# Kernel tuning notes

Hardware: AMD Instinct MI355X
Metric: run time of the kernel (lower is better)

Reference implementation:

```python
import jax, jax.numpy as jnp
import numpy as np

NUM_NEIGHBORS = 3
EPS = 1e-10
B, N1, N2 = 8, 8192, 2048
C1, C2 = 256, 512


def setup_inputs() -> dict:
    key = jax.random.key(0)
    k1, k2, k3, k4 = jax.random.split(key, 4)
    return {
        "query_xyz": jax.random.uniform(k1, (B, 3, N1), dtype=jnp.float32),
        "key_xyz": jax.random.uniform(k2, (B, 3, N2), dtype=jnp.float32),
        "query_feature": jax.random.normal(k3, (B, C1, N1), dtype=jnp.float32),
        "key_feature": jax.random.normal(k4, (B, C2, N2), dtype=jnp.float32),
    }


def reference(query_xyz, key_xyz, query_feature, key_feature):
    # q: (B, N1, 3), k: (B, N2, 3)
    q = jnp.swapaxes(query_xyz, 1, 2)
    k = jnp.swapaxes(key_xyz, 1, 2)
    # squared pairwise distances (B, N1, N2) via ||q||^2 + ||k||^2 - 2 q.k
    d2 = (
        jnp.sum(q * q, axis=-1, keepdims=True)
        + jnp.sum(k * k, axis=-1)[:, None, :]
        - 2.0 * jnp.einsum("bnd,bmd->bnm", q, k)
    )
    # k nearest neighbors (smallest distances)
    neg_d, index = jax.lax.top_k(-d2, NUM_NEIGHBORS)  # (B, N1, K)
    distance = jnp.maximum(-neg_d, EPS)
    inv_distance = 1.0 / distance
    weight = inv_distance / jnp.sum(inv_distance, axis=2, keepdims=True)
    # torch.no_grad() block -> constants w.r.t. autodiff
    weight = jax.lax.stop_gradient(weight)
    index = jax.lax.stop_gradient(index)
    # gather key features: feat_t (B, N2, C2) -> gathered (B, N1, K, C2)
    feat_t = jnp.swapaxes(key_feature, 1, 2)
    batch_idx = jnp.arange(feat_t.shape[0])[:, None, None]
    gathered = feat_t[batch_idx, index]
    # inverse-distance weighted sum -> (B, C2, N1)
    interpolated = jnp.einsum("bnk,bnkc->bcn", weight, gathered)
    return jnp.concatenate([interpolated, query_feature], axis=1)
```

## Files before the change

kernel.cpp:

```cpp
#include <hip/hip_runtime.h>

#define NB 8
#define N1 8192
#define N2 2048
#define C1 256
#define C2 512
#define CO 768
#define CCH 4

typedef float f2 __attribute__((ext_vector_type(2)));
typedef float f4 __attribute__((ext_vector_type(4)));


#define NRM2(X, Y, Z) ({                                                   \
    float _s, _t;                                                          \
    asm("v_mul_f32 %0, %2, %2\n\t"                                         \
        "v_mul_f32 %1, %3, %3\n\t"                                         \
        "v_add_f32 %0, %0, %1\n\t"                                         \
        "v_mul_f32 %1, %4, %4\n\t"                                         \
        "v_add_f32 %0, %0, %1"                                             \
        : "=&v"(_s), "=&v"(_t) : "v"(X), "v"(Y), "v"(Z));                  \
    _s; })

#define PKD2(X01, Y01, Z01, K01, QXD, QYD, QZD, QQD, M2) ({                \
    f2 _d, _s;                                                             \
    asm("v_pk_mul_f32 %0, %2, %6\n\t"           \
        "v_pk_fma_f32 %0, %3, %7, %0\n\t"       \
        "v_pk_fma_f32 %0, %4, %8, %0\n\t"       \
        "v_pk_add_f32 %1, %5, %9\n\t"           \
        "v_pk_fma_f32 %0, %0, %10, %1"          \
        : "=&v"(_d), "=&v"(_s)                                             \
        : "v"(X01), "v"(Y01), "v"(Z01), "v"(K01),                          \
          "v"(QXD), "v"(QYD), "v"(QZD), "v"(QQD), "v"(M2));                \
    _d; })

#define INS(S, D2, J) do {                                                 \
        float _v = (D2);                                                   \
        if (_v < b2##S) {                                                  \
            bool c0 = _v < b0##S, c1 = _v < b1##S;                         \
            b2##S = c1 ? b1##S : _v;                                       \
            i2##S = c1 ? i1##S : (J);                                      \
            b1##S = c0 ? b0##S : (c1 ? _v : b1##S);                        \
            i1##S = c0 ? i0##S : (c1 ? (J) : i1##S);                       \
            b0##S = c0 ? _v : b0##S;                                       \
            i0##S = c0 ? (J) : i0##S;                                      \
        } } while (0)

__global__ __launch_bounds__(256) void pack_keys(
    const float* __restrict__ kxyz,
    float4* __restrict__ keys4)
{
    const int b = blockIdx.x >> 3;
    const int j = (blockIdx.x & 7) * 256 + threadIdx.x;
    const float* kb = kxyz + (size_t)b * 3 * N2;
    float x = kb[j], y = kb[N2 + j], z = kb[2 * N2 + j];
    keys4[(size_t)b * N2 + j] = make_float4(x, y, z, NRM2(x, y, z));
}

__global__ __launch_bounds__(512, 4) void knn_scan(
    const float* __restrict__ qxyz,
    const float4* __restrict__ keys4,
    const float* __restrict__ qfeat,
    int*   __restrict__ nn_idx,
    float* __restrict__ nn_w,
    float* __restrict__ out)
{
    __shared__ __align__(16) float skx[N2];
    __shared__ __align__(16) float sky[N2];
    __shared__ __align__(16) float skz[N2];
    __shared__ __align__(16) float skk[N2];
    __shared__ float pd[8][128][3];
    __shared__ int   pi[8][128][3];

    const int b    = blockIdx.x >> 6;
    const int tile = blockIdx.x & 63;
    const int n0   = tile * 128;
    const int tid  = threadIdx.x;
    const int w    = tid >> 6, lane = tid & 63;

    const float4* kb4 = keys4 + (size_t)b * N2;
    for (int j = tid; j < N2; j += 512) {
        float4 k4 = kb4[j];
        skx[j] = k4.x; sky[j] = k4.y; skz[j] = k4.z; skk[j] = k4.w;
    }
    __syncthreads();

    const int na = n0 + lane, nb = n0 + 64 + lane;
    const float* qb = qxyz + (size_t)b * 3 * N1;
    const float qxA = qb[na], qyA = qb[N1 + na], qzA = qb[2 * N1 + na];
    const float qxB = qb[nb], qyB = qb[N1 + nb], qzB = qb[2 * N1 + nb];
    const float qqA = NRM2(qxA, qyA, qzA);
    const float qqB = NRM2(qxB, qyB, qzB);

    f2 qxdA, qydA, qzdA, qqdA, qxdB, qydB, qzdB, qqdB, m2;
    qxdA.x = qxA; qxdA.y = qxA;  qydA.x = qyA; qydA.y = qyA;
    qzdA.x = qzA; qzdA.y = qzA;  qqdA.x = qqA; qqdA.y = qqA;
    qxdB.x = qxB; qxdB.y = qxB;  qydB.x = qyB; qydB.y = qyB;
    qzdB.x = qzB; qzdB.y = qzB;  qqdB.x = qqB; qqdB.y = qqB;
    m2.x = -2.0f; m2.y = -2.0f;

    float b0A = 3.4e38f, b1A = 3.4e38f, b2A = 3.4e38f;
    float b0B = 3.4e38f, b1B = 3.4e38f, b2B = 3.4e38f;
    int   i0A = 0, i1A = 0, i2A = 0, i0B = 0, i1B = 0, i2B = 0;

    const int jlo = w * (N2 / 8);
    #pragma unroll 4
    for (int g = 0; g < (N2 / 8) / 4; ++g) {
        const int jb = jlo + g * 4;
        f4 x4 = *(const f4*)&skx[jb];
        f4 y4 = *(const f4*)&sky[jb];
        f4 z4 = *(const f4*)&skz[jb];
        f4 k4 = *(const f4*)&skk[jb];
        f2 dA01 = PKD2(x4.xy, y4.xy, z4.xy, k4.xy, qxdA, qydA, qzdA, qqdA, m2);
        f2 dA23 = PKD2(x4.zw, y4.zw, z4.zw, k4.zw, qxdA, qydA, qzdA, qqdA, m2);
        f2 dB01 = PKD2(x4.xy, y4.xy, z4.xy, k4.xy, qxdB, qydB, qzdB, qqdB, m2);
        f2 dB23 = PKD2(x4.zw, y4.zw, z4.zw, k4.zw, qxdB, qydB, qzdB, qqdB, m2);
        INS(A, dA01.x, jb);     INS(A, dA01.y, jb + 1);
        INS(A, dA23.x, jb + 2); INS(A, dA23.y, jb + 3);
        INS(B, dB01.x, jb);     INS(B, dB01.y, jb + 1);
        INS(B, dB23.x, jb + 2); INS(B, dB23.y, jb + 3);
    }

    pd[w][lane][0] = b0A; pd[w][lane][1] = b1A; pd[w][lane][2] = b2A;
    pi[w][lane][0] = i0A; pi[w][lane][1] = i1A; pi[w][lane][2] = i2A;
    pd[w][64 + lane][0] = b0B; pd[w][64 + lane][1] = b1B; pd[w][64 + lane][2] = b2B;
    pi[w][64 + lane][0] = i0B; pi[w][64 + lane][1] = i1B; pi[w][64 + lane][2] = i2B;
    __syncthreads();

    if (tid < 128) {
        float m0 = 3.4e38f, m1 = 3.4e38f, m2s = 3.4e38f;
        int   j0 = 0, j1 = 0, j2 = 0;
        #pragma unroll
        for (int c = 0; c < 8; ++c) {
            #pragma unroll
            for (int s = 0; s < 3; ++s) {
                float d = pd[c][tid][s];
                int   i = pi[c][tid][s];
                if (d < m2s) {
                    bool c0 = d < m0, c1 = d < m1;
                    m2s = c1 ? m1 : d;               j2 = c1 ? j1 : i;
                    m1 = c0 ? m0 : (c1 ? d : m1);    j1 = c0 ? j0 : (c1 ? i : j1);
                    m0 = c0 ? d : m0;                j0 = c0 ? i  : j0;
                }
            }
        }
        float d0f = fmaxf(m0, 1e-10f), d1f = fmaxf(m1, 1e-10f), d2f = fmaxf(m2s, 1e-10f);
        float v0 = __fdiv_rn(1.0f, d0f), v1 = __fdiv_rn(1.0f, d1f), v2 = __fdiv_rn(1.0f, d2f);
        float s  = __fadd_rn(__fadd_rn(v0, v1), v2);
        const size_t g = (size_t)b * N1 + n0 + tid;
        *(int4*)  &nn_idx[g * 4] = make_int4(j0, j1, j2, 0);
        *(float4*)&nn_w  [g * 4] = make_float4(__fdiv_rn(v0, s), __fdiv_rn(v1, s),
                                               __fdiv_rn(v2, s), 0.0f);
    }

    const float4* qsrc = (const float4*)(qfeat + (size_t)b * C1 * N1);
    float4*       qdst = (float4*)(out + (size_t)b * CO * N1 + (size_t)C2 * N1);
    #pragma unroll
    for (int k = 0; k < 16; ++k) {
        const size_t r = (size_t)tile * 8192 + (size_t)k * 512 + tid;
        qdst[r] = qsrc[r];
    }
}

__global__ __launch_bounds__(256) void interp4(
    const float* __restrict__ kfeat,
    const int*   __restrict__ nn_idx,
    const float* __restrict__ nn_w,
    float* __restrict__ out)
{
    __shared__ __align__(16) float4 skf[N2];
    const int b     = blockIdx.x & 7;
    const int cg    = blockIdx.x >> 3;
    const int cbase = cg * CCH;
    const int tid   = threadIdx.x;

    const float* kf = kfeat + (size_t)b * C2 * N2 + (size_t)cbase * N2;
    for (int j = tid; j < N2; j += 256) {
        skf[j] = make_float4(kf[j], kf[N2 + j], kf[2 * N2 + j], kf[3 * N2 + j]);
    }
    __syncthreads();

    const int*   ib = nn_idx + (size_t)b * N1 * 4;
    const float* wb = nn_w   + (size_t)b * N1 * 4;
    float* ob = out + (size_t)b * CO * N1;

    #pragma unroll 4
    for (int t = 0; t < N1 / 256; ++t) {
        const int n = t * 256 + tid;
        const int4   iv = *(const int4*)  &ib[(size_t)n * 4];
        const float4 wv = *(const float4*)&wb[(size_t)n * 4];
        const float4 f0 = skf[iv.x];
        const float4 f1 = skf[iv.y];
        const float4 f2v = skf[iv.z];
        ob[(size_t)(cbase + 0) * N1 + n] =
            fmaf(wv.z, f2v.x, fmaf(wv.y, f1.x, __fmul_rn(wv.x, f0.x)));
        ob[(size_t)(cbase + 1) * N1 + n] =
            fmaf(wv.z, f2v.y, fmaf(wv.y, f1.y, __fmul_rn(wv.x, f0.y)));
        ob[(size_t)(cbase + 2) * N1 + n] =
            fmaf(wv.z, f2v.z, fmaf(wv.y, f1.z, __fmul_rn(wv.x, f0.z)));
        ob[(size_t)(cbase + 3) * N1 + n] =
            fmaf(wv.z, f2v.w, fmaf(wv.y, f1.w, __fmul_rn(wv.x, f0.w)));
    }
}

extern "C" void kernel_launch(void* const* d_in, const int* in_sizes, int n_in,
                              void* d_out, int out_size, void* d_ws, size_t ws_size,
                              hipStream_t stream) {
    const float* qxyz  = (const float*)d_in[0];
    const float* kxyz  = (const float*)d_in[1];
    const float* qfeat = (const float*)d_in[2];
    const float* kfeat = (const float*)d_in[3];
    float* out = (float*)d_out;

    float*  ws     = (float*)d_ws;
    float4* keys4  = (float4*)ws;
    int*    nn_idx = (int*)(ws + (size_t)4 * NB * N2);
    float*  nn_w   = ws + (size_t)4 * NB * N2 + (size_t)4 * NB * N1;

    pack_keys<<<NB * (N2 / 256), 256, 0, stream>>>(kxyz, keys4);
    knn_scan<<<NB * (N1 / 128), 512, 0, stream>>>(qxyz, keys4, qfeat,
                                                  nn_idx, nn_w, out);
    interp4<<<NB * (C2 / CCH), 256, 0, stream>>>(kfeat, nn_idx, nn_w, out);
}
```

Measured before the change: 112.3 us.

## Fuse key packing into KNN scan and make top-3 insertion branchless

```diff
diff --git a/kernel.cpp b/kernel.cpp
--- a/kernel.cpp
+++ b/kernel.cpp
@@ -36,30 +36,18 @@
 
 #define INS(S, D2, J) do {                                                 \
         float _v = (D2);                                                   \
-        if (_v < b2##S) {                                                  \
-            bool c0 = _v < b0##S, c1 = _v < b1##S;                         \
-            b2##S = c1 ? b1##S : _v;                                       \
-            i2##S = c1 ? i1##S : (J);                                      \
-            b1##S = c0 ? b0##S : (c1 ? _v : b1##S);                        \
-            i1##S = c0 ? i0##S : (c1 ? (J) : i1##S);                       \
-            b0##S = c0 ? _v : b0##S;                                       \
-            i0##S = c0 ? (J) : i0##S;                                      \
-        } } while (0)
-
-__global__ __launch_bounds__(256) void pack_keys(
-    const float* __restrict__ kxyz,
-    float4* __restrict__ keys4)
-{
-    const int b = blockIdx.x >> 3;
-    const int j = (blockIdx.x & 7) * 256 + threadIdx.x;
-    const float* kb = kxyz + (size_t)b * 3 * N2;
-    float x = kb[j], y = kb[N2 + j], z = kb[2 * N2 + j];
-    keys4[(size_t)b * N2 + j] = make_float4(x, y, z, NRM2(x, y, z));
-}
+        bool c2 = _v < b2##S, c1 = _v < b1##S, c0 = _v < b0##S;            \
+        i2##S = c2 ? (c1 ? i1##S : (J)) : i2##S;                           \
+        b2##S = c2 ? (c1 ? b1##S : _v) : b2##S;                            \
+        i1##S = c0 ? i0##S : (c1 ? (J) : i1##S);                           \
+        b1##S = c0 ? b0##S : (c1 ? _v : b1##S);                            \
+        i0##S = c0 ? (J) : i0##S;                                          \
+        b0##S = c0 ? _v : b0##S;                                           \
+    } while (0)
 
 __global__ __launch_bounds__(512, 4) void knn_scan(
     const float* __restrict__ qxyz,
-    const float4* __restrict__ keys4,
+    const float* __restrict__ kxyz,
     const float* __restrict__ qfeat,
     int*   __restrict__ nn_idx,
     float* __restrict__ nn_w,
@@ -78,10 +66,11 @@
     const int tid  = threadIdx.x;
     const int w    = tid >> 6, lane = tid & 63;
 
-    const float4* kb4 = keys4 + (size_t)b * N2;
+    const float* kb = kxyz + (size_t)b * 3 * N2;
     for (int j = tid; j < N2; j += 512) {
-        float4 k4 = kb4[j];
-        skx[j] = k4.x; sky[j] = k4.y; skz[j] = k4.z; skk[j] = k4.w;
+        float x = kb[j], y = kb[N2 + j], z = kb[2 * N2 + j];
+        skx[j] = x; sky[j] = y; skz[j] = z;
+        skk[j] = NRM2(x, y, z);
     }
     __syncthreads();
 
@@ -212,13 +201,10 @@
     const float* kfeat = (const float*)d_in[3];
     float* out = (float*)d_out;
 
-    float*  ws     = (float*)d_ws;
-    float4* keys4  = (float4*)ws;
-    int*    nn_idx = (int*)(ws + (size_t)4 * NB * N2);
-    float*  nn_w   = ws + (size_t)4 * NB * N2 + (size_t)4 * NB * N1;
-
-    pack_keys<<<NB * (N2 / 256), 256, 0, stream>>>(kxyz, keys4);
-    knn_scan<<<NB * (N1 / 128), 512, 0, stream>>>(qxyz, keys4, qfeat,
+    int*   nn_idx = (int*)d_ws;
+    float* nn_w   = (float*)d_ws + (size_t)4 * NB * N1;
+
+    knn_scan<<<NB * (N1 / 128), 512, 0, stream>>>(qxyz, kxyz, qfeat,
                                                   nn_idx, nn_w, out);
     interp4<<<NB * (C2 / CCH), 256, 0, stream>>>(kfeat, nn_idx, nn_w, out);
 }
```

After: 117.6 us. 4.7% more time.

## Transpose key features to point-major and gather rows per query tile

Applied to the files above, without the earlier changes.

```diff
diff --git a/kernel.cpp b/kernel.cpp
--- a/kernel.cpp
+++ b/kernel.cpp
@@ -6,7 +6,6 @@
 #define C1 256
 #define C2 512
 #define CO 768
-#define CCH 4
 
 typedef float f2 __attribute__((ext_vector_type(2)));
 typedef float f4 __attribute__((ext_vector_type(4)));
@@ -46,15 +45,39 @@
             i0##S = c0 ? (J) : i0##S;                                      \
         } } while (0)
 
-__global__ __launch_bounds__(256) void pack_keys(
+__global__ __launch_bounds__(256) void prep(
     const float* __restrict__ kxyz,
-    float4* __restrict__ keys4)
+    const float* __restrict__ kfeat,
+    float4* __restrict__ keys4,
+    float*  __restrict__ ft)
 {
-    const int b = blockIdx.x >> 3;
-    const int j = (blockIdx.x & 7) * 256 + threadIdx.x;
-    const float* kb = kxyz + (size_t)b * 3 * N2;
-    float x = kb[j], y = kb[N2 + j], z = kb[2 * N2 + j];
-    keys4[(size_t)b * N2 + j] = make_float4(x, y, z, NRM2(x, y, z));
+    __shared__ float t[64][65];
+    if (blockIdx.x < 2048) {
+        const int jb = (blockIdx.x & 31) * 64;
+        const int cb = ((blockIdx.x >> 5) & 7) * 64;
+        const int b  = blockIdx.x >> 8;
+        const float* src = kfeat + (size_t)b * C2 * N2;
+        float* dst = ft + (size_t)b * N2 * C2;
+        const int lj = threadIdx.x & 63, hi = threadIdx.x >> 6;
+        #pragma unroll
+        for (int k = 0; k < 16; ++k) {
+            const int c = hi * 16 + k;
+            t[c][lj] = src[(size_t)(cb + c) * N2 + jb + lj];
+        }
+        __syncthreads();
+        #pragma unroll
+        for (int k = 0; k < 16; ++k) {
+            const int j = hi * 16 + k;
+            dst[(size_t)(jb + j) * C2 + cb + lj] = t[lj][j];
+        }
+    } else {
+        const int bid = blockIdx.x - 2048;
+        const int b = bid >> 3;
+        const int j = (bid & 7) * 256 + threadIdx.x;
+        const float* kb = kxyz + (size_t)b * 3 * N2;
+        float x = kb[j], y = kb[N2 + j], z = kb[2 * N2 + j];
+        keys4[(size_t)b * N2 + j] = make_float4(x, y, z, NRM2(x, y, z));
+    }
 }
 
 __global__ __launch_bounds__(512, 4) void knn_scan(
@@ -162,44 +185,51 @@
     }
 }
 
-__global__ __launch_bounds__(256) void interp4(
-    const float* __restrict__ kfeat,
+__global__ __launch_bounds__(256) void interp7(
+    const float* __restrict__ ft,
     const int*   __restrict__ nn_idx,
     const float* __restrict__ nn_w,
     float* __restrict__ out)
 {
-    __shared__ __align__(16) float4 skf[N2];
-    const int b     = blockIdx.x & 7;
-    const int cg    = blockIdx.x >> 3;
-    const int cbase = cg * CCH;
-    const int tid   = threadIdx.x;
-
-    const float* kf = kfeat + (size_t)b * C2 * N2 + (size_t)cbase * N2;
-    for (int j = tid; j < N2; j += 256) {
-        skf[j] = make_float4(kf[j], kf[N2 + j], kf[2 * N2 + j], kf[3 * N2 + j]);
+    __shared__ float  stile[64][65];
+    __shared__ int4   nni[64];
+    __shared__ float4 nnw[64];
+    const int b    = blockIdx.x & 7;
+    const int tile = blockIdx.x >> 3;
+    const int n0   = tile * 64;
+    const int tid  = threadIdx.x;
+    const int w    = tid >> 6, lane = tid & 63;
+
+    if (tid < 64) {
+        const size_t g = (size_t)b * N1 + n0 + tid;
+        nni[tid] = *(const int4*)  &nn_idx[g * 4];
+        nnw[tid] = *(const float4*)&nn_w  [g * 4];
     }
     __syncthreads();
 
-    const int*   ib = nn_idx + (size_t)b * N1 * 4;
-    const float* wb = nn_w   + (size_t)b * N1 * 4;
+    const float* ftb = ft + (size_t)b * N2 * C2;
     float* ob = out + (size_t)b * CO * N1;
 
-    #pragma unroll 4
-    for (int t = 0; t < N1 / 256; ++t) {
-        const int n = t * 256 + tid;
-        const int4   iv = *(const int4*)  &ib[(size_t)n * 4];
-        const float4 wv = *(const float4*)&wb[(size_t)n * 4];
-        const float4 f0 = skf[iv.x];
-        const float4 f1 = skf[iv.y];
-        const float4 f2v = skf[iv.z];
-        ob[(size_t)(cbase + 0) * N1 + n] =
-            fmaf(wv.z, f2v.x, fmaf(wv.y, f1.x, __fmul_rn(wv.x, f0.x)));
-        ob[(size_t)(cbase + 1) * N1 + n] =
-            fmaf(wv.z, f2v.y, fmaf(wv.y, f1.y, __fmul_rn(wv.x, f0.y)));
-        ob[(size_t)(cbase + 2) * N1 + n] =
-            fmaf(wv.z, f2v.z, fmaf(wv.y, f1.z, __fmul_rn(wv.x, f0.z)));
-        ob[(size_t)(cbase + 3) * N1 + n] =
-            fmaf(wv.z, f2v.w, fmaf(wv.y, f1.w, __fmul_rn(wv.x, f0.w)));
+    for (int cg = 0; cg < 8; ++cg) {
+        const int cbase = cg * 64;
+        #pragma unroll 4
+        for (int t = 0; t < 16; ++t) {
+            const int q = w * 16 + t;
+            const int4   iv = nni[q];
+            const float4 wv = nnw[q];
+            const float f0 = ftb[(size_t)iv.x * C2 + cbase + lane];
+            const float f1 = ftb[(size_t)iv.y * C2 + cbase + lane];
+            const float f2l = ftb[(size_t)iv.z * C2 + cbase + lane];
+            stile[lane][q] = fmaf(wv.z, f2l, fmaf(wv.y, f1, __fmul_rn(wv.x, f0)));
+        }
+        __syncthreads();
+        #pragma unroll
+        for (int k = 0; k < 16; ++k) {
+            const int idx = k * 256 + tid;
+            const int c = idx >> 6, q = idx & 63;
+            ob[(size_t)(cbase + c) * N1 + n0 + q] = stile[c][q];
+        }
+        __syncthreads();
     }
 }
 
@@ -213,12 +243,13 @@
     float* out = (float*)d_out;
 
     float*  ws     = (float*)d_ws;
-    float4* keys4  = (float4*)ws;
-    int*    nn_idx = (int*)(ws + (size_t)4 * NB * N2);
-    float*  nn_w   = ws + (size_t)4 * NB * N2 + (size_t)4 * NB * N1;
-
-    pack_keys<<<NB * (N2 / 256), 256, 0, stream>>>(kxyz, keys4);
+    float*  ft     = ws;
+    float4* keys4  = (float4*)(ws + (size_t)NB * N2 * C2);
+    int*    nn_idx = (int*)(ws + (size_t)NB * N2 * C2 + 4 * NB * N2);
+    float*  nn_w   = ws + (size_t)NB * N2 * C2 + 4 * NB * N2 + 4 * NB * N1;
+
+    prep<<<2048 + NB * (N2 / 256), 256, 0, stream>>>(kxyz, kfeat, keys4, ft);
     knn_scan<<<NB * (N1 / 128), 512, 0, stream>>>(qxyz, keys4, qfeat,
                                                   nn_idx, nn_w, out);
-    interp4<<<NB * (C2 / CCH), 256, 0, stream>>>(kfeat, nn_idx, nn_w, out);
-}
+    interp7<<<NB * (N1 / 64), 256, 0, stream>>>(ft, nn_idx, nn_w, out);
+}
```

Measured after the change: 131.8 us. 1.17x slower.
